# Kernel tuning notes

Measured on AMD Instinct MI355X. Metric: run time of the kernel, lower is better.

The kernel has to match this reference:

```python
import jax, jax.numpy as jnp
import numpy as np

H = W = 56
WS = 7            # window size
SHIFT = 3
HEADS = 6
DIM = 192
N = WS * WS       # tokens per window (49)
NW = (H // WS) * (W // WS)  # windows per image (64)
EPS = 1e-5


def _rel_pos_index():
    coords = np.stack(np.meshgrid(np.arange(WS), np.arange(WS), indexing='ij'))
    cf = coords.reshape(2, -1)
    rel = (cf[:, :, None] - cf[:, None, :]).transpose(1, 2, 0)
    rel[:, :, 0] += WS - 1
    rel[:, :, 1] += WS - 1
    rel[:, :, 0] *= 2 * WS - 1
    return rel.sum(-1).astype(np.int32)  # [N, N]


def _attn_mask():
    img = np.zeros([1, H, W, 1], dtype=np.float32)
    slices = (slice(0, -WS), slice(-WS, -SHIFT), slice(-SHIFT, None))
    cnt = 0
    for hs in slices:
        for ws_ in slices:
            img[:, hs, ws_, :] = cnt
            cnt += 1
    m = img.reshape(1, H // WS, WS, W // WS, WS, 1).transpose(0, 1, 3, 2, 4, 5)
    m = m.reshape(-1, N)                      # [nW, N]
    diff = m[:, None, :] - m[:, :, None]
    return np.where(diff != 0, -100.0, 0.0).astype(np.float32)  # [nW, N, N]

_RPI = _rel_pos_index()
_MASK = _attn_mask()


def _ln(x, g, b):
    mu = jnp.mean(x, axis=-1, keepdims=True)
    var = jnp.mean(jnp.square(x - mu), axis=-1, keepdims=True)
    return (x - mu) * jax.lax.rsqrt(var + EPS) * g + b


def setup_inputs() -> dict:
    key = jax.random.key(0)
    ks = jax.random.split(key, 12)
    C, Hd = DIM, DIM * 4
    s = lambda n: 1.0 / np.sqrt(n)
    return {
        'x': jax.random.normal(ks[0], (32, H * W, C), jnp.float32),
        'norm1_g': jnp.ones((C,), jnp.float32),
        'norm1_b': jnp.zeros((C,), jnp.float32),
        'qkv_w': jax.random.normal(ks[1], (C, 3 * C), jnp.float32) * s(C),
        'qkv_b': jnp.zeros((3 * C,), jnp.float32),
        'bias_table': jax.random.normal(ks[2], ((2 * WS - 1) ** 2, HEADS), jnp.float32) * 0.02,
        'proj_w': jax.random.normal(ks[3], (C, C), jnp.float32) * s(C),
        'proj_b': jnp.zeros((C,), jnp.float32),
        'norm2_g': jnp.ones((C,), jnp.float32),
        'norm2_b': jnp.zeros((C,), jnp.float32),
        'fc1_w': jax.random.normal(ks[4], (C, Hd), jnp.float32) * s(C),
        'fc1_b': jnp.zeros((Hd,), jnp.float32),
        'fc2_w': jax.random.normal(ks[5], (Hd, C), jnp.float32) * s(Hd),
        'fc2_b': jnp.zeros((C,), jnp.float32),
    }


def reference(x, norm1_g, norm1_b, qkv_w, qkv_b, bias_table, proj_w, proj_b,
              norm2_g, norm2_b, fc1_w, fc1_b, fc2_w, fc2_b):
    B, L, C = x.shape
    hd = C // HEADS
    scale = hd ** -0.5

    shortcut = x
    h = _ln(x, norm1_g, norm1_b).reshape(B, H, W, C)
    h = jnp.roll(h, (-SHIFT, -SHIFT), axis=(1, 2))

    # window partition -> [B*nW, N, C]
    h = h.reshape(B, H // WS, WS, W // WS, WS, C).transpose(0, 1, 3, 2, 4, 5)
    xw = h.reshape(B * NW, N, C)

    qkv = (xw @ qkv_w + qkv_b).reshape(B * NW, N, 3, HEADS, hd)
    q, k, v = jnp.moveaxis(qkv, 2, 0)                 # each [B*nW, N, H, d]
    q = jnp.swapaxes(q, 1, 2) * scale                 # [B*nW, H, N, d]
    k = jnp.swapaxes(k, 1, 2)
    v = jnp.swapaxes(v, 1, 2)

    attn = jnp.einsum('whnd,whmd->whnm', q, k)        # [B*nW, H, N, N]
    bias = bias_table[jnp.asarray(_RPI).reshape(-1)].reshape(N, N, HEADS)
    attn = attn + jnp.transpose(bias, (2, 0, 1))[None]
    mask = jnp.asarray(_MASK)                         # [nW, N, N]
    attn = attn.reshape(B, NW, HEADS, N, N) + mask[None, :, None]
    attn = jax.nn.softmax(attn.reshape(B * NW, HEADS, N, N), axis=-1)

    out = jnp.einsum('whnm,whmd->whnd', attn, v)      # [B*nW, H, N, d]
    out = jnp.swapaxes(out, 1, 2).reshape(B * NW, N, C)
    out = out @ proj_w + proj_b

    # window reverse -> [B, H, W, C]
    out = out.reshape(B, H // WS, W // WS, WS, WS, C).transpose(0, 1, 3, 2, 4, 5)
    out = out.reshape(B, H, W, C)
    out = jnp.roll(out, (SHIFT, SHIFT), axis=(1, 2)).reshape(B, L, C)

    x = shortcut + out
    hmlp = _ln(x, norm2_g, norm2_b)
    hmlp = jax.nn.gelu(hmlp @ fc1_w + fc1_b, approximate=False) @ fc2_w + fc2_b
    return x + hmlp
```

## Files before the change

### kernel.cpp

```cpp
#include <hip/hip_runtime.h>
#include <hip/hip_bf16.h>
#include <math.h>

static constexpr int CB     = 32;
static constexpr int CH     = 56;
static constexpr int CW     = 56;
static constexpr int CC     = 192;
static constexpr int CSHIFT = 3;
static constexpr int CN     = 49;
static constexpr int CNW    = 64;
static constexpr int CL     = CH * CW;
static constexpr int CM     = CB * CNW * CN;
static constexpr int CHID   = 768;

typedef __attribute__((ext_vector_type(8))) __bf16 bf16x8;
typedef __attribute__((ext_vector_type(4))) float  f32x4;

__device__ __forceinline__ float bfu2f(unsigned short u) {
  union { unsigned i; float f; } c; c.i = (unsigned)u << 16; return c.f;
}
__device__ __forceinline__ unsigned short f2bu(float f) {
  __hip_bfloat16 b = __float2bfloat16(f);
  return *(unsigned short*)&b;
}
__device__ __forceinline__ float gelu_fast(float v) {
  float e = __expf(-1.702f * v);
  return __fdividef(v, 1.0f + e);
}

#define GLOAD16(g, l) __builtin_amdgcn_global_load_lds( \
    (__attribute__((address_space(1))) void*)(g),       \
    (__attribute__((address_space(3))) void*)(l), 16, 0, 0)

__global__ __launch_bounds__(256)
void prep_kernel(const float* __restrict__ qkv_w, const float* __restrict__ proj_w,
                 const float* __restrict__ fc1_w, const float* __restrict__ fc2_w,
                 const float* __restrict__ btab,
                 __hip_bfloat16* __restrict__ wq, __hip_bfloat16* __restrict__ wp,
                 __hip_bfloat16* __restrict__ w1, __hip_bfloat16* __restrict__ w2,
                 float* __restrict__ bias2)
{
  int idx = blockIdx.x * 256 + threadIdx.x;
  if (idx < 110592) {
    int k = idx / 576, n = idx - k * 576;
    wq[n * 192 + k] = __float2bfloat16(qkv_w[idx]);
    return;
  }
  idx -= 110592;
  if (idx < 36864) {
    int k = idx / 192, n = idx - k * 192;
    wp[n * 192 + k] = __float2bfloat16(proj_w[idx]);
    return;
  }
  idx -= 36864;
  if (idx < 147456) {
    int k = idx / 768, n = idx - k * 768;
    w1[n * 192 + k] = __float2bfloat16(fc1_w[idx]);
    return;
  }
  idx -= 147456;
  if (idx < 147456) {
    int k = idx / 192, n = idx - k * 192;
    w2[n * 768 + k] = __float2bfloat16(fc2_w[idx]);
    return;
  }
  idx -= 147456;
  if (idx < 98304) {
    int j = idx & 63, i = (idx >> 6) & 63;
    int rest = idx >> 12;
    int h = rest % 6, wt = rest / 6;
    float val;
    if (i >= 49 || j >= 49) {
      val = -INFINITY;
    } else {
      int ti = i / 7, ci = i - ti * 7;
      int tj = j / 7, cj = j - tj * 7;
      val = btab[((ti - tj + 6) * 13 + (ci - cj + 6)) * 6 + h];
      int hri = (wt & 2) ? ((ti < 4) ? 1 : 2) : 0;
      int hci = (wt & 1) ? ((ci < 4) ? 1 : 2) : 0;
      int hrj = (wt & 2) ? ((tj < 4) ? 1 : 2) : 0;
      int hcj = (wt & 1) ? ((cj < 4) ? 1 : 2) : 0;
      if (hri * 3 + hci != hrj * 3 + hcj) val -= 100.0f;
    }
    bias2[idx] = val;
  }
}

template<bool ROLL, bool BIN>
__global__ __launch_bounds__(256)
void ln_kernel(const void* __restrict__ xin, const float* __restrict__ gamma,
               const float* __restrict__ beta, __hip_bfloat16* __restrict__ out)
{
  const int wid = threadIdx.x >> 6, lane = threadIdx.x & 63;
  const int m = blockIdx.x * 4 + wid;
  size_t src;
  if (ROLL) {
    int b   = m / (CNW * CN);
    int rem = m - b * (CNW * CN);
    int nw  = rem / CN, t = rem - nw * CN;
    int wr = nw >> 3, wc = nw & 7;
    int ti = t / 7, tj = t - ti * 7;
    int sr = wr * 7 + ti + CSHIFT; if (sr >= CH) sr -= CH;
    int sc = wc * 7 + tj + CSHIFT; if (sc >= CW) sc -= CW;
    src = ((size_t)b * CL + (size_t)sr * CW + sc) * CC;
  } else {
    src = (size_t)m * CC;
  }
  const float* xf = (const float*)xin;
  const unsigned short* xb = (const unsigned short*)xin;
  float v0 = BIN ? bfu2f(xb[src + lane      ]) : xf[src + lane      ];
  float v1 = BIN ? bfu2f(xb[src + lane + 64 ]) : xf[src + lane + 64 ];
  float v2 = BIN ? bfu2f(xb[src + lane + 128]) : xf[src + lane + 128];
  float s  = v0 + v1 + v2;
  float sq = v0 * v0 + v1 * v1 + v2 * v2;
  #pragma unroll
  for (int off = 32; off; off >>= 1) { s += __shfl_xor(s, off); sq += __shfl_xor(sq, off); }
  const float mu  = s * (1.0f / CC);
  const float inv = rsqrtf(sq * (1.0f / CC) - mu * mu + 1e-5f);
  const size_t dst = (size_t)m * CC;
  out[dst + lane      ] = __float2bfloat16((v0 - mu) * inv * gamma[lane      ] + beta[lane      ]);
  out[dst + lane + 64 ] = __float2bfloat16((v1 - mu) * inv * gamma[lane + 64 ] + beta[lane + 64 ]);
  out[dst + lane + 128] = __float2bfloat16((v2 - mu) * inv * gamma[lane + 128] + beta[lane + 128]);
}

template<int K, int N, int BN, int MODE>
__global__ __launch_bounds__(256)
void gemm_mfma(const __hip_bfloat16* __restrict__ Ain, const __hip_bfloat16* __restrict__ Wt,
               const float* __restrict__ bias, void* __restrict__ Outv,
               const void* __restrict__ residv)
{
  constexpr int NT = BN / 32;
  __shared__ short As[128 * 64];
  __shared__ short Bs[BN * 64];

  const int tid  = threadIdx.x;
  const int lane = tid & 63, wid = tid >> 6;

  const int nbx = N / BN;
  const int nwg = nbx * gridDim.y;
  const int wg  = blockIdx.y * nbx + blockIdx.x;
  const int swz = (wg & 7) * (nwg >> 3) + (wg >> 3);
  const int row0 = (swz / nbx) * 128, col0 = (swz % nbx) * BN;

  const int wm = wid >> 1, wn = wid & 1;
  const int lr = lane & 15, lg = lane >> 4;

  const short* A  = (const short*)Ain;
  const short* W  = (const short*)Wt;

  f32x4 acc[4][NT] = {};

  #pragma unroll
  for (int kk = 0; kk < K; kk += 64) {
    #pragma unroll
    for (int it = 0; it < 4; ++it) {
      int c = it * 256 + tid;
      int row = c >> 3, slot = c & 7;
      int kg = (slot ^ (row & 7)) * 8;
      GLOAD16(A + (size_t)(row0 + row) * K + kk + kg, As + c * 8);
    }
    #pragma unroll
    for (int it = 0; it < BN / 32; ++it) {
      int c = it * 256 + tid;
      int row = c >> 3, slot = c & 7;
      int kg = (slot ^ (row & 7)) * 8;
      GLOAD16(W + (size_t)(col0 + row) * K + kk + kg, Bs + c * 8);
    }
    __syncthreads();

    #pragma unroll
    for (int kh = 0; kh < 2; ++kh) {
      const int sb = kh * 4 + lg;
      bf16x8 bfr[NT];
      #pragma unroll
      for (int nt = 0; nt < NT; ++nt) {
        int br = wn * (BN / 2) + nt * 16 + lr;
        bfr[nt] = *(const bf16x8*)(Bs + br * 64 + (sb ^ (br & 7)) * 8);
      }
      #pragma unroll
      for (int m = 0; m < 4; ++m) {
        int ar = wm * 64 + m * 16 + lr;
        bf16x8 afr = *(const bf16x8*)(As + ar * 64 + (sb ^ (ar & 7)) * 8);
        #pragma unroll
        for (int nt = 0; nt < NT; ++nt)
          acc[m][nt] = __builtin_amdgcn_mfma_f32_16x16x32_bf16(afr, bfr[nt], acc[m][nt], 0, 0, 0);
      }
    }
    __syncthreads();
  }

  const int colA = col0 + wn * (BN / 2) + lr;
  float bv[NT];
  #pragma unroll
  for (int nt = 0; nt < NT; ++nt) bv[nt] = bias[colA + nt * 16];

  #pragma unroll
  for (int m = 0; m < 4; ++m) {
    #pragma unroll
    for (int r = 0; r < 4; ++r) {
      const int mrow = row0 + wm * 64 + m * 16 + lg * 4 + r;
      if (MODE == 0) {
        __hip_bfloat16* O = (__hip_bfloat16*)Outv;
        const size_t rr = (size_t)mrow * N + colA;
        #pragma unroll
        for (int nt = 0; nt < NT; ++nt)
          O[rr + nt * 16] = __float2bfloat16(acc[m][nt][r] + bv[nt]);
      } else if (MODE == 1 || MODE == 4) {
        int b = mrow / (CNW * CN);
        int rem = mrow - b * (CNW * CN);
        int nw = rem / CN, t = rem - nw * CN;
        int wr = nw >> 3, wc = nw & 7;
        int ti = t / 7, tj = t - ti * 7;
        int dr = wr * 7 + ti + CSHIFT; if (dr >= CH) dr -= CH;
        int dc = wc * 7 + tj + CSHIFT; if (dc >= CW) dc -= CW;
        const size_t dst = ((size_t)b * CL + (size_t)dr * CW + dc) * CC + colA;
        const float* resid = (const float*)residv;
        if (MODE == 1) {
          float* O = (float*)Outv;
          #pragma unroll
          for (int nt = 0; nt < NT; ++nt)
            O[dst + nt * 16] = resid[dst + nt * 16] + acc[m][nt][r] + bv[nt];
        } else {
          __hip_bfloat16* O = (__hip_bfloat16*)Outv;
          #pragma unroll
          for (int nt = 0; nt < NT; ++nt)
            O[dst + nt * 16] = __float2bfloat16(resid[dst + nt * 16] + acc[m][nt][r] + bv[nt]);
        }
      } else if (MODE == 2) {
        __hip_bfloat16* O = (__hip_bfloat16*)Outv;
        const size_t rr = (size_t)mrow * N + colA;
        #pragma unroll
        for (int nt = 0; nt < NT; ++nt)
          O[rr + nt * 16] = __float2bfloat16(gelu_fast(acc[m][nt][r] + bv[nt]));
      } else if (MODE == 3) {
        float* O = (float*)Outv;
        const float* resid = (const float*)residv;
        const size_t rr = (size_t)mrow * N + colA;
        #pragma unroll
        for (int nt = 0; nt < NT; ++nt)
          O[rr + nt * 16] = resid[rr + nt * 16] + acc[m][nt][r] + bv[nt];
      } else {
        float* O = (float*)Outv;
        const unsigned short* resid = (const unsigned short*)residv;
        const size_t rr = (size_t)mrow * N + colA;
        #pragma unroll
        for (int nt = 0; nt < NT; ++nt)
          O[rr + nt * 16] = bfu2f(resid[rr + nt * 16]) + acc[m][nt][r] + bv[nt];
      }
    }
  }
}

__global__ __launch_bounds__(64)
void attn_mfma_kernel(const __hip_bfloat16* __restrict__ qkv,
                      const float* __restrict__ bias2,
                      __hip_bfloat16* __restrict__ attnout)
{
  __shared__ unsigned short VT[32 * 72];

  const int bid = blockIdx.x;
  const int w = bid / 6, h = bid - (bid / 6) * 6;
  const int lane = threadIdx.x;
  const int lr = lane & 15, lg = lane >> 4;
  const int nw = w & 63;
  const int wt = (((nw >> 3) == 7) ? 2 : 0) + (((nw & 7) == 7) ? 1 : 0);
  const unsigned short* Q = (const unsigned short*)qkv;
  const size_t rowbase = (size_t)w * 49 * 576;
  const float scale = 0.17677669529663687f;

  for (int e = lane; e < 196; e += 64) {
    int t = e % 49, c = e / 49;
    uint4 v = *(const uint4*)(Q + rowbase + (size_t)t * 576 + 384 + h * 32 + c * 8);
    unsigned va[4] = {v.x, v.y, v.z, v.w};
    #pragma unroll
    for (int q = 0; q < 4; ++q) {
      VT[(c * 8 + q * 2    ) * 72 + t] = (unsigned short)(va[q] & 0xffff);
      VT[(c * 8 + q * 2 + 1) * 72 + t] = (unsigned short)(va[q] >> 16);
    }
  }
  for (int e = lane; e < 32 * 15; e += 64) {
    int d = e / 15, t = 49 + e - (e / 15) * 15;
    VT[d * 72 + t] = 0;
  }

  bf16x8 qf[4], kf[4];
  #pragma unroll
  for (int it = 0; it < 4; ++it) {
    int tok = it * 16 + lr; if (tok > 48) tok = 48;
    qf[it] = *(const bf16x8*)(Q + rowbase + (size_t)tok * 576 + h * 32 + lg * 8);
  }
  #pragma unroll
  for (int jt = 0; jt < 4; ++jt) {
    int tok = jt * 16 + lr; if (tok > 48) tok = 48;
    kf[jt] = *(const bf16x8*)(Q + rowbase + (size_t)tok * 576 + 192 + h * 32 + lg * 8);
  }

  f32x4 acc[4][4] = {};
  __builtin_amdgcn_s_setprio(1);
  #pragma unroll
  for (int jt = 0; jt < 4; ++jt)
    #pragma unroll
    for (int it = 0; it < 4; ++it)
      acc[jt][it] = __builtin_amdgcn_mfma_f32_16x16x32_bf16(kf[jt], qf[it], acc[jt][it], 0, 0, 0);
  __builtin_amdgcn_s_setprio(0);

  __syncthreads();

  bf16x8 vb[2][2];
  #pragma unroll
  for (int ks = 0; ks < 2; ++ks)
    #pragma unroll
    for (int nt = 0; nt < 2; ++nt)
      vb[ks][nt] = *(const bf16x8*)&VT[(nt * 16 + lr) * 72 + ks * 32 + lg * 8];

  const float* brow = bias2 + ((size_t)(wt * 6 + h) * 64) * 64;
  const int src0 = lr + ((lg & 1) << 5);
  f32x4 o[4][2] = {};

  #pragma unroll
  for (int it = 0; it < 4; ++it) {
    const int i = it * 16 + lr;
    float s[4][4];
    #pragma unroll
    for (int jt = 0; jt < 4; ++jt) {
      float4 bv = *(const float4*)(brow + (size_t)i * 64 + jt * 16 + lg * 4);
      s[jt][0] = fmaf(acc[jt][it][0], scale, bv.x);
      s[jt][1] = fmaf(acc[jt][it][1], scale, bv.y);
      s[jt][2] = fmaf(acc[jt][it][2], scale, bv.z);
      s[jt][3] = fmaf(acc[jt][it][3], scale, bv.w);
    }
    float mx = s[0][0];
    #pragma unroll
    for (int jt = 0; jt < 4; ++jt)
      #pragma unroll
      for (int r = 0; r < 4; ++r) mx = fmaxf(mx, s[jt][r]);
    mx = fmaxf(mx, __shfl_xor(mx, 16));
    mx = fmaxf(mx, __shfl_xor(mx, 32));
    float sum = 0.0f;
    #pragma unroll
    for (int jt = 0; jt < 4; ++jt)
      #pragma unroll
      for (int r = 0; r < 4; ++r) { s[jt][r] = __expf(s[jt][r] - mx); sum += s[jt][r]; }
    sum += __shfl_xor(sum, 16);
    sum += __shfl_xor(sum, 32);
    const float inv = 1.0f / sum;

    unsigned wpk[4][2];
    #pragma unroll
    for (int jt = 0; jt < 4; ++jt) {
      wpk[jt][0] = (unsigned)f2bu(s[jt][0] * inv) | ((unsigned)f2bu(s[jt][1] * inv) << 16);
      wpk[jt][1] = (unsigned)f2bu(s[jt][2] * inv) | ((unsigned)f2bu(s[jt][3] * inv) << 16);
    }
    #pragma unroll
    for (int ks = 0; ks < 2; ++ks) {
      union { bf16x8 v; unsigned u[4]; } pa;
      #pragma unroll
      for (int wd = 0; wd < 4; ++wd) {
        const int src = src0 + ((wd >> 1) << 4);
        unsigned v0 = (unsigned)__shfl((int)wpk[ks * 2    ][wd & 1], src);
        unsigned v1 = (unsigned)__shfl((int)wpk[ks * 2 + 1][wd & 1], src);
        pa.u[wd] = (lg & 2) ? v1 : v0;
      }
      __builtin_amdgcn_s_setprio(1);
      o[it][0] = __builtin_amdgcn_mfma_f32_16x16x32_bf16(pa.v, vb[ks][0], o[it][0], 0, 0, 0);
      o[it][1] = __builtin_amdgcn_mfma_f32_16x16x32_bf16(pa.v, vb[ks][1], o[it][1], 0, 0, 0);
      __builtin_amdgcn_s_setprio(0);
    }
  }

  #pragma unroll
  for (int it = 0; it < 4; ++it) {
    #pragma unroll
    for (int r = 0; r < 4; ++r) {
      int i = it * 16 + lg * 4 + r;
      if (i < 49) {
        size_t dst = ((size_t)w * 49 + i) * 192 + h * 32;
        attnout[dst + lr]      = __float2bfloat16(o[it][0][r]);
        attnout[dst + 16 + lr] = __float2bfloat16(o[it][1][r]);
      }
    }
  }
}

extern "C" void kernel_launch(void* const* d_in, const int* in_sizes, int n_in,
                              void* d_out, int out_size, void* d_ws, size_t ws_size,
                              hipStream_t stream)
{
  const float* x        = (const float*)d_in[0];
  const float* n1g      = (const float*)d_in[1];
  const float* n1b      = (const float*)d_in[2];
  const float* qkv_w    = (const float*)d_in[3];
  const float* qkv_b    = (const float*)d_in[4];
  const float* btab     = (const float*)d_in[5];
  const float* proj_w   = (const float*)d_in[6];
  const float* proj_b   = (const float*)d_in[7];
  const float* n2g      = (const float*)d_in[8];
  const float* n2b      = (const float*)d_in[9];
  const float* fc1_w    = (const float*)d_in[10];
  const float* fc1_b    = (const float*)d_in[11];
  const float* fc2_w    = (const float*)d_in[12];
  const float* fc2_b    = (const float*)d_in[13];
  float* out = (float*)d_out;

  char* ws = (char*)d_ws;
  const size_t szA = (size_t)CM * CC * 2;
  const size_t szB = (size_t)CM * CHID * 2;
  const size_t szW = (size_t)(110592 + 36864 + 147456 + 147456) * 2;
  const size_t szb2 = (size_t)98304 * 4;
  __hip_bfloat16* bufA = (__hip_bfloat16*)ws;
  __hip_bfloat16* bufB = (__hip_bfloat16*)(ws + szA);
  __hip_bfloat16* wq   = (__hip_bfloat16*)(ws + szA + szB);
  __hip_bfloat16* wp   = wq + 576 * 192;
  __hip_bfloat16* w1   = wp + 192 * 192;
  __hip_bfloat16* w2   = w1 + 768 * 192;
  float* bias2         = (float*)(w2 + 192 * 768);
  __hip_bfloat16* bufC = (__hip_bfloat16*)(ws + szA + szB + szW + szb2);

  const bool bf16trunk = ws_size >= szA + szB + szW + szb2 + szA;

  const int prep_total = 110592 + 36864 + 147456 + 147456 + 98304;
  prep_kernel<<<(prep_total + 255) / 256, 256, 0, stream>>>(
      qkv_w, proj_w, fc1_w, fc2_w, btab, wq, wp, w1, w2, bias2);

  ln_kernel<true, false><<<CM / 4, 256, 0, stream>>>(x, n1g, n1b, bufA);
  gemm_mfma<192, 576, 96, 0><<<dim3(576 / 96, CM / 128), 256, 0, stream>>>(bufA, wq, qkv_b, bufB, nullptr);
  attn_mfma_kernel<<<2048 * 6, 64, 0, stream>>>(bufB, bias2, bufA);

  if (bf16trunk) {
    gemm_mfma<192, 192, 64, 4><<<dim3(192 / 64, CM / 128), 256, 0, stream>>>(bufA, wp, proj_b, bufC, x);
    ln_kernel<false, true><<<CM / 4, 256, 0, stream>>>(bufC, n2g, n2b, bufA);
    gemm_mfma<192, CHID, 128, 2><<<dim3(CHID / 128, CM / 128), 256, 0, stream>>>(bufA, w1, fc1_b, bufB, nullptr);
    gemm_mfma<CHID, 192, 64, 5><<<dim3(192 / 64, CM / 128), 256, 0, stream>>>(bufB, w2, fc2_b, out, bufC);
  } else {
    gemm_mfma<192, 192, 64, 1><<<dim3(192 / 64, CM / 128), 256, 0, stream>>>(bufA, wp, proj_b, out, x);
    ln_kernel<false, false><<<CM / 4, 256, 0, stream>>>(out, n2g, n2b, bufA);
    gemm_mfma<192, CHID, 128, 2><<<dim3(CHID / 128, CM / 128), 256, 0, stream>>>(bufA, w1, fc1_b, bufB, nullptr);
    gemm_mfma<CHID, 192, 64, 3><<<dim3(192 / 64, CM / 128), 256, 0, stream>>>(bufB, w2, fc2_b, out, out);
  }
}
```

Before: 316.7 us.

## Double-buffer GEMM shared tiles with K-step of 32 and new swizzle

Restructures the MFMA GEMM main loop to use two shared-memory buffers with a K-chunk of 32 instead of one buffer of 64. The next chunk is prefetched while the current one is computed, which cuts one barrier per iteration. The LDS swizzle is redesigned for 4 slots per row. This trades more iterations and smaller chunks for overlap of global loads with MFMA work.

```diff
diff --git a/kernel.cpp b/kernel.cpp
--- a/kernel.cpp
+++ b/kernel.cpp
@@ -129,9 +129,11 @@
                const float* __restrict__ bias, void* __restrict__ Outv,
                const void* __restrict__ residv)
 {
-  constexpr int NT = BN / 32;
-  __shared__ short As[128 * 64];
-  __shared__ short Bs[BN * 64];
+  constexpr int NT  = BN / 32;
+  constexpr int ACH = 128 * 32;
+  constexpr int BCH = BN * 32;
+  __shared__ short As[2][ACH];
+  __shared__ short Bs[2][BCH];
 
   const int tid  = threadIdx.x;
   const int lane = tid & 63, wid = tid >> 6;
@@ -144,47 +146,53 @@
 
   const int wm = wid >> 1, wn = wid & 1;
   const int lr = lane & 15, lg = lane >> 4;
+  const int s0 = (lr & 3) ^ ((lr >> 2) & 3);
 
   const short* A  = (const short*)Ain;
   const short* W  = (const short*)Wt;
 
+  auto stage = [&](int buf, int kk) {
+    #pragma unroll
+    for (int it = 0; it < 2; ++it) {
+      int c = it * 256 + tid;
+      int row = c >> 2, slot = c & 3;
+      int kg = (slot ^ (row & 3) ^ ((row >> 2) & 3)) * 8;
+      GLOAD16(A + (size_t)(row0 + row) * K + kk + kg, &As[buf][c * 8]);
+    }
+    #pragma unroll
+    for (int it = 0; it < (BCH / 8 + 255) / 256; ++it) {
+      int c = it * 256 + tid;
+      if ((BCH / 8) % 256 == 0 || c < BCH / 8) {
+        int row = c >> 2, slot = c & 3;
+        int kg = (slot ^ (row & 3) ^ ((row >> 2) & 3)) * 8;
+        GLOAD16(W + (size_t)(col0 + row) * K + kk + kg, &Bs[buf][c * 8]);
+      }
+    }
+  };
+
   f32x4 acc[4][NT] = {};
 
-  #pragma unroll
-  for (int kk = 0; kk < K; kk += 64) {
-    #pragma unroll
-    for (int it = 0; it < 4; ++it) {
-      int c = it * 256 + tid;
-      int row = c >> 3, slot = c & 7;
-      int kg = (slot ^ (row & 7)) * 8;
-      GLOAD16(A + (size_t)(row0 + row) * K + kk + kg, As + c * 8);
-    }
-    #pragma unroll
-    for (int it = 0; it < BN / 32; ++it) {
-      int c = it * 256 + tid;
-      int row = c >> 3, slot = c & 7;
-      int kg = (slot ^ (row & 7)) * 8;
-      GLOAD16(W + (size_t)(col0 + row) * K + kk + kg, Bs + c * 8);
-    }
-    __syncthreads();
-
-    #pragma unroll
-    for (int kh = 0; kh < 2; ++kh) {
-      const int sb = kh * 4 + lg;
-      bf16x8 bfr[NT];
+  stage(0, 0);
+  __syncthreads();
+
+  #pragma unroll
+  for (int ks = 0; ks < K / 32; ++ks) {
+    const int cur = ks & 1;
+    if (ks + 1 < K / 32) stage(cur ^ 1, (ks + 1) * 32);
+
+    bf16x8 bfr[NT];
+    #pragma unroll
+    for (int nt = 0; nt < NT; ++nt) {
+      int br = wn * (BN / 2) + nt * 16 + lr;
+      bfr[nt] = *(const bf16x8*)&Bs[cur][br * 32 + (lg ^ s0) * 8];
+    }
+    #pragma unroll
+    for (int m = 0; m < 4; ++m) {
+      int ar = wm * 64 + m * 16 + lr;
+      bf16x8 afr = *(const bf16x8*)&As[cur][ar * 32 + (lg ^ s0) * 8];
       #pragma unroll
-      for (int nt = 0; nt < NT; ++nt) {
-        int br = wn * (BN / 2) + nt * 16 + lr;
-        bfr[nt] = *(const bf16x8*)(Bs + br * 64 + (sb ^ (br & 7)) * 8);
-      }
-      #pragma unroll
-      for (int m = 0; m < 4; ++m) {
-        int ar = wm * 64 + m * 16 + lr;
-        bf16x8 afr = *(const bf16x8*)(As + ar * 64 + (sb ^ (ar & 7)) * 8);
-        #pragma unroll
-        for (int nt = 0; nt < NT; ++nt)
-          acc[m][nt] = __builtin_amdgcn_mfma_f32_16x16x32_bf16(afr, bfr[nt], acc[m][nt], 0, 0, 0);
-      }
+      for (int nt = 0; nt < NT; ++nt)
+        acc[m][nt] = __builtin_amdgcn_mfma_f32_16x16x32_bf16(afr, bfr[nt], acc[m][nt], 0, 0, 0);
     }
     __syncthreads();
   }
```

After: 336.2 us. 1.06x slower.
